# Performance work log

Measured on AMD Instinct MI355X. Metric: run time of the kernel, lower is better.

Reference implementation:

```python
import jax, jax.numpy as jnp
import numpy as np

N_QUBITS = 12
N_LAYERS = 6
N_CLASSES = 10
BATCH = 4096


def _rot_matrix(phi, theta, omega):
    # PennyLane Rot(phi, theta, omega) = RZ(omega) @ RY(theta) @ RZ(phi)
    ct = jnp.cos(theta / 2).astype(jnp.complex64)
    st = jnp.sin(theta / 2).astype(jnp.complex64)
    ep = jnp.exp(-0.5j * (phi + omega)).astype(jnp.complex64)  # e^{-i(phi+omega)/2}
    em = jnp.exp(-0.5j * (phi - omega)).astype(jnp.complex64)  # e^{-i(phi-omega)/2}
    row0 = jnp.stack([ep * ct, -jnp.conj(em) * st])
    row1 = jnp.stack([em * st, jnp.conj(ep) * ct])
    return jnp.stack([row0, row1])  # [2, 2] complex64


def _apply_1q(state, U, q):
    # state: [B] + [2]*n ; apply 2x2 gate U on qubit axis q
    s = jnp.moveaxis(state, q + 1, -1)
    s = jnp.einsum('...i,ji->...j', s, U)
    return jnp.moveaxis(s, -1, q + 1)


def _apply_cnot(state, c, t):
    # flip target axis where control bit == 1
    s = jnp.moveaxis(state, (c + 1, t + 1), (1, 2))
    s = jnp.concatenate([s[:, :1], jnp.flip(s[:, 1:2], axis=2)], axis=1)
    return jnp.moveaxis(s, (1, 2), (c + 1, t + 1))


def _pauliz_signs(n):
    idx = np.arange(2 ** n)
    bits = (idx[None, :] >> (n - 1 - np.arange(n))[:, None]) & 1  # [n, 2^n]
    return jnp.asarray(1.0 - 2.0 * bits, dtype=jnp.float32)


def _quantum_forward(x, q_params):
    B, n = x.shape
    # rotation encoding: RY(x_q)|0> = [cos(x/2), sin(x/2)] -> product state
    c = jnp.cos(x / 2)
    s = jnp.sin(x / 2)
    state = jnp.ones((B, 1), dtype=jnp.complex64)
    for q in range(n):
        amp = jnp.stack([c[:, q], s[:, q]], axis=-1).astype(jnp.complex64)  # [B, 2]
        state = (state[:, :, None] * amp[:, None, :]).reshape(B, -1)
    state = state.reshape((B,) + (2,) * n)
    # StronglyEntanglingLayers: per-layer Rot on every wire, then CNOT ring with range r
    for l in range(N_LAYERS):
        for q in range(n):
            U = _rot_matrix(q_params[l, q, 0], q_params[l, q, 1], q_params[l, q, 2])
            state = _apply_1q(state, U, q)
        r = (l % (n - 1)) + 1
        for q in range(n):
            state = _apply_cnot(state, q, (q + r) % n)
    probs = (jnp.abs(state) ** 2).reshape(B, -1).astype(jnp.float32)  # [B, 2^n]
    signs = _pauliz_signs(n)  # [n, 2^n]
    return probs @ signs.T  # PauliZ expvals, [B, n]


def setup_inputs() -> dict:
    key = jax.random.key(0)
    k1, k2, k3, k4 = jax.random.split(key, 4)
    x = jax.random.normal(k1, (BATCH, N_QUBITS), dtype=jnp.float32)
    q_params = 0.01 * jax.random.normal(k2, (N_LAYERS, N_QUBITS, 3), dtype=jnp.float32)
    lim = 1.0 / np.sqrt(N_QUBITS)
    fc_w = jax.random.uniform(k3, (N_CLASSES, N_QUBITS), jnp.float32, -lim, lim)
    fc_b = jax.random.uniform(k4, (N_CLASSES,), jnp.float32, -lim, lim)
    return {"x": x, "q_params": q_params, "fc_w": fc_w, "fc_b": fc_b}


def reference(x, q_params, fc_w, fc_b):
    expvals = _quantum_forward(x, q_params)  # [B, n_qubits]
    return expvals @ fc_w.T + fc_b  # logits [B, n_classes]
```

## Files before the change

kernel.cpp:

```cpp
#include <hip/hip_runtime.h>
#include <hip/hip_fp16.h>

#define NQ 12
#define NL 6
#define NC 10
#define DIM 4096
#define TPB 256
#define NPASS 18

typedef _Float16 half8_t __attribute__((ext_vector_type(8)));
typedef float f32x4 __attribute__((ext_vector_type(4)));
typedef unsigned u32;

struct PassT {
    u32 colL[4];
    u32 colW[2];
    u32 colT[2];
    u32 colS[4];
};
struct QCArgs {
    PassT P[NPASS];
    u32 GcolI[8], AcolI[8];
    u32 svoIlog[16], svoIaddr[16];
    u32 tidMask[NQ];
    u32 tab16[NQ];
};

__device__ __forceinline__ u32 packh2(float a, float b) {
    __half2 h;
    h.x = __float2half(a);
    h.y = __float2half(b);
    return __builtin_bit_cast(u32, h);
}
__device__ __forceinline__ float r16(float v) { return __half2float(__float2half(v)); }

__global__ __launch_bounds__(TPB) void prep_k(const float* __restrict__ qp, uint4* __restrict__ ws)
{
    __shared__ float4 gmat[NL * NQ];
    const unsigned tid = threadIdx.x;
    const unsigned lane = tid & 63;
    const unsigned wv = tid >> 6;

    if (tid < NL * NQ) {
        float phi = qp[tid * 3 + 0];
        float th  = qp[tid * 3 + 1];
        float om  = qp[tid * 3 + 2];
        float st_, ct, sa, ca, sb, cb;
        sincosf(0.5f * th, &st_, &ct);
        sincosf(0.5f * (phi + om), &sa, &ca);
        sincosf(0.5f * (phi - om), &sb, &cb);
        gmat[tid] = make_float4(ca * ct, -sa * ct, cb * st_, -sb * st_);
    }
    __syncthreads();

    const int i16 = lane & 15;
    const int sb0 = (int)(lane >> 4) * 4;
    for (int k = (int)wv; k < NPASS; k += 4) {
        const int gb = (k / 3) * NQ + (k % 3) * 4;
        u32 fH[4], fL[4];
        #pragma unroll
        for (int jj = 0; jj < 4; ++jj) {
            int s = sb0 + jj;
            float cre = 1.0f, cim = 0.0f;
            #pragma unroll
            for (int g = 0; g < 4; ++g) {
                float4 gq = gmat[gb + g];
                int ib = (i16 >> g) & 1, sb2 = (s >> g) & 1;
                float er, ei;
                if (ib == 0 && sb2 == 0)      { er =  gq.x; ei =  gq.y; }
                else if (ib == 0 && sb2 == 1) { er = -gq.z; ei =  gq.w; }
                else if (ib == 1 && sb2 == 0) { er =  gq.z; ei =  gq.w; }
                else                          { er =  gq.x; ei = -gq.y; }
                float nre = cre * er - cim * ei;
                float nim = cre * ei + cim * er;
                cre = nre; cim = nim;
            }
            float mi = -cim;
            fH[jj] = packh2(cre, mi);
            fL[jj] = packh2(cre - r16(cre), mi - r16(mi));
        }
        uint4 h = make_uint4(fH[0], fH[1], fH[2], fH[3]);
        uint4 l = make_uint4(fL[0], fL[1], fL[2], fL[3]);
        uint4 hI, lI;
        hI.x = ((h.x << 16) | (h.x >> 16)) ^ 0x8000u;
        hI.y = ((h.y << 16) | (h.y >> 16)) ^ 0x8000u;
        hI.z = ((h.z << 16) | (h.z >> 16)) ^ 0x8000u;
        hI.w = ((h.w << 16) | (h.w >> 16)) ^ 0x8000u;
        lI.x = ((l.x << 16) | (l.x >> 16)) ^ 0x8000u;
        lI.y = ((l.y << 16) | (l.y >> 16)) ^ 0x8000u;
        lI.z = ((l.z << 16) | (l.z >> 16)) ^ 0x8000u;
        lI.w = ((l.w << 16) | (l.w >> 16)) ^ 0x8000u;
        ws[0 * 1152 + k * 64 + lane] = h;
        ws[1 * 1152 + k * 64 + lane] = l;
        ws[2 * 1152 + k * 64 + lane] = hI;
        ws[3 * 1152 + k * 64 + lane] = lI;
    }
}

__global__ __launch_bounds__(TPB, 4) void qsim_k(
    const float* __restrict__ x,
    const float* __restrict__ fcw, const float* __restrict__ fcb,
    float* __restrict__ out, int B, const uint4* __restrict__ ws, QCArgs K)
{
    __shared__ u32 stamp[DIM];
    __shared__ float csn[NQ], snn[NQ];
    __shared__ float zred[4 * NQ];
    __shared__ float zfin[NQ];

    const unsigned tid = threadIdx.x;
    const unsigned lane = tid & 63;
    const unsigned wv = tid >> 6;
    const int blk = blockIdx.x;

    if (tid < NQ) {
        float s, c;
        sincosf(0.5f * x[(size_t)blk * NQ + tid], &s, &c);
        csn[tid] = c; snn[tid] = s;
    }
    __syncthreads();

    {
        float csr[NQ], snr[NQ];
        #pragma unroll
        for (int p = 0; p < NQ; ++p) { csr[p] = csn[11 - p]; snr[p] = snn[11 - p]; }
        u32 G = 0, A0 = 0;
        #pragma unroll
        for (int b = 0; b < 8; ++b) {
            u32 mneg = (u32)(-(int)((tid >> b) & 1u));
            G  ^= mneg & K.GcolI[b];
            A0 ^= mneg & K.AcolI[b];
        }
        #pragma unroll
        for (int s = 0; s < 16; ++s) {
            u32 idx = G ^ K.svoIlog[s];
            float amp = 1.0f;
            #pragma unroll
            for (int p = 0; p < NQ; ++p)
                amp *= ((idx >> p) & 1) ? snr[p] : csr[p];
            *(u32*)((char*)stamp + (A0 ^ K.svoIaddr[s])) = packh2(amp, 0.0f);
        }
    }

    float pr[16];

    #pragma unroll 1
    for (int k = 0; k < NPASS; ++k) {
        uint4 fh  = ws[0 * 1152 + k * 64 + lane];
        uint4 fl  = ws[1 * 1152 + k * 64 + lane];
        uint4 fhI = ws[2 * 1152 + k * 64 + lane];
        uint4 flI = ws[3 * 1152 + k * 64 + lane];
        half8_t AreH = __builtin_bit_cast(half8_t, fh);
        half8_t AreL = __builtin_bit_cast(half8_t, fl);
        half8_t AimH = __builtin_bit_cast(half8_t, fhI);
        half8_t AimL = __builtin_bit_cast(half8_t, flI);

        __syncthreads();
        const PassT& P = K.P[k];

        u32 A = 0;
        A ^= (lane & 1u)  ? P.colL[0] : 0u;
        A ^= (lane & 2u)  ? P.colL[1] : 0u;
        A ^= (lane & 4u)  ? P.colL[2] : 0u;
        A ^= (lane & 8u)  ? P.colL[3] : 0u;
        A ^= (lane & 16u) ? P.colS[2] : 0u;
        A ^= (lane & 32u) ? P.colS[3] : 0u;
        A ^= (wv & 1u) ? P.colW[0] : 0u;
        A ^= (wv & 2u) ? P.colW[1] : 0u;
        const u32 o1 = P.colS[0], o2 = P.colS[1], o3 = o1 ^ o2;
        const u32 t1 = P.colT[0], t2 = P.colT[1];
        const u32 tf[4] = {0u, t1, t2, t1 ^ t2};

        #pragma unroll
        for (int t = 0; t < 4; ++t) {
            u32 At = A ^ tf[t];
            u32 b0 = *(const u32*)((const char*)stamp + At);
            u32 b1 = *(const u32*)((const char*)stamp + (At ^ o1));
            u32 b2 = *(const u32*)((const char*)stamp + (At ^ o2));
            u32 b3 = *(const u32*)((const char*)stamp + (At ^ o3));
            half8_t Bf = __builtin_bit_cast(half8_t, make_uint4(b0, b1, b2, b3));
            f32x4 zc = {0.0f, 0.0f, 0.0f, 0.0f};
            f32x4 Dre = __builtin_amdgcn_mfma_f32_16x16x32_f16(
                AreH, Bf, __builtin_amdgcn_mfma_f32_16x16x32_f16(AreL, Bf, zc, 0, 0, 0), 0, 0, 0);
            f32x4 Dim = __builtin_amdgcn_mfma_f32_16x16x32_f16(
                AimH, Bf, __builtin_amdgcn_mfma_f32_16x16x32_f16(AimL, Bf, zc, 0, 0, 0), 0, 0, 0);
            if (k < NPASS - 1) {
                *(u32*)((char*)stamp + At)        = packh2(Dre[0], Dim[0]);
                *(u32*)((char*)stamp + (At ^ o1)) = packh2(Dre[1], Dim[1]);
                *(u32*)((char*)stamp + (At ^ o2)) = packh2(Dre[2], Dim[2]);
                *(u32*)((char*)stamp + (At ^ o3)) = packh2(Dre[3], Dim[3]);
            } else {
                pr[t * 4 + 0] = fmaf(Dre[0], Dre[0], Dim[0] * Dim[0]);
                pr[t * 4 + 1] = fmaf(Dre[1], Dre[1], Dim[1] * Dim[1]);
                pr[t * 4 + 2] = fmaf(Dre[2], Dre[2], Dim[2] * Dim[2]);
                pr[t * 4 + 3] = fmaf(Dre[3], Dre[3], Dim[3] * Dim[3]);
            }
        }
    }

    float z[NQ];
    #pragma unroll
    for (int q = 0; q < NQ; ++q) {
        float base = (__popc(K.tidMask[q] & tid) & 1) ? -1.0f : 1.0f;
        u32 tb = K.tab16[q];
        float acc = 0.0f;
        #pragma unroll
        for (int idx = 0; idx < 16; ++idx) {
            float sgn = ((tb >> idx) & 1u) ? -base : base;
            acc = fmaf(sgn, pr[idx], acc);
        }
        z[q] = acc;
    }
    #pragma unroll
    for (int q = 0; q < NQ; ++q) {
        float v = z[q];
        #pragma unroll
        for (int o = 1; o < 64; o <<= 1) v += __shfl_xor(v, o, 64);
        z[q] = v;
    }
    if ((tid & 63) == 0) {
        #pragma unroll
        for (int q = 0; q < NQ; ++q) zred[wv * NQ + q] = z[q];
    }
    __syncthreads();
    if (tid < NQ)
        zfin[tid] = zred[tid] + zred[NQ + tid] + zred[2 * NQ + tid] + zred[3 * NQ + tid];
    __syncthreads();

    if (tid < NC) {
        float acc = fcb[tid];
        #pragma unroll
        for (int q = 0; q < NQ; ++q) acc = fmaf(fcw[tid * NQ + q], zfin[q], acc);
        out[(size_t)blk * NC + tid] = acc;
    }
}

static void inv12(const unsigned Ain[12], unsigned Ai[12]) {
    unsigned M[12], I[12];
    for (int i = 0; i < 12; ++i) { M[i] = Ain[i]; I[i] = 1u << i; }
    for (int c = 0; c < 12; ++c) {
        int pr = -1;
        for (int r2 = c; r2 < 12; ++r2) if ((M[r2] >> c) & 1u) { pr = r2; break; }
        unsigned tm = M[c]; M[c] = M[pr]; M[pr] = tm;
        tm = I[c]; I[c] = I[pr]; I[pr] = tm;
        for (int r2 = 0; r2 < 12; ++r2)
            if (r2 != c && ((M[r2] >> c) & 1u)) { M[r2] ^= M[c]; I[r2] ^= I[c]; }
    }
    for (int i = 0; i < 12; ++i) Ai[i] = I[i];
}
static unsigned lcg(unsigned& s) { s = s * 1664525u + 1013904223u; return s >> 8; }
static int pc(unsigned v) { return __builtin_popcount(v); }

extern "C" void kernel_launch(void* const* d_in, const int* in_sizes, int n_in,
                              void* d_out, int out_size, void* d_ws, size_t ws_size,
                              hipStream_t stream) {
    const float* x    = (const float*)d_in[0];
    const float* qp   = (const float*)d_in[1];
    const float* fc_w = (const float*)d_in[2];
    const float* fc_b = (const float*)d_in[3];
    float* out = (float*)d_out;
    int B = in_sizes[0] / NQ;

    unsigned L[12];
    for (int i = 0; i < 12; ++i) L[i] = 1u << i;
    static unsigned vAll[NPASS][4], rAll[NPASS][4], vcAll[NPASS][16];
    static int posAll[NPASS][8];
    for (int l = 0; l < NL; ++l) {
        unsigned Linv[12];
        inv12(L, Linv);
        for (int m = 0; m < 3; ++m) {
            int k = l * 3 + m;
            for (int j = 0; j < 4; ++j) {
                int qq = 4 * m + j, bb = 11 - qq;
                rAll[k][j] = L[bb];
                unsigned vv = 0;
                for (int i = 0; i < 12; ++i) vv |= ((Linv[i] >> bb) & 1u) << i;
                vAll[k][j] = vv;
            }
            unsigned w[4]; int piv[4];
            for (int j = 0; j < 4; ++j) {
                w[j] = vAll[k][j];
                for (int k2 = 0; k2 < j; ++k2)
                    if ((w[j] >> piv[k2]) & 1u) w[j] ^= w[k2];
                piv[j] = __builtin_ctz(w[j]);
            }
            bool ispiv[12] = {};
            for (int j = 0; j < 4; ++j) ispiv[piv[j]] = true;
            int c = 0;
            for (int pos = 0; pos < 12; ++pos)
                if (!ispiv[pos]) posAll[k][c++] = pos;
            for (int s = 0; s < 16; ++s) {
                unsigned vc = 0;
                for (int j = 0; j < 4; ++j) if ((s >> j) & 1) vc ^= vAll[k][j];
                vcAll[k][s] = vc;
            }
        }
        int rr = l + 1;
        for (int q = 0; q < 12; ++q) {
            int tq = (q + rr) % 12;
            L[11 - tq] ^= L[11 - q];
        }
    }
    unsigned rfin[12];
    for (int q = 0; q < 12; ++q) rfin[q] = L[11 - q];

    unsigned labels[12];
    unsigned seed = 0x5EED321u;
    auto lab5 = [&](unsigned v) -> unsigned {
        unsigned r = 0;
        for (int pos = 0; pos < 12; ++pos) if ((v >> pos) & 1u) r ^= labels[pos];
        return r & 31u;
    };
    bool okAll = false;
    for (int att = 0; att < 300000 && !okAll; ++att) {
        for (int i = 0; i < 12; ++i) labels[i] = 1u + (lcg(seed) % 31u);
        okAll = true;
        for (int k = 0; k < NPASS && okAll; ++k) {
            unsigned Labj[4];
            for (int j = 0; j < 4; ++j) Labj[j] = lab5(vAll[k][j]);
            unsigned ech[5], low[5]; int rk = 0;
            unsigned v2l = Labj[2];
            if (v2l) { ech[rk] = v2l; low[rk] = v2l & (0u - v2l); ++rk; }
            int got = 0;
            for (int b = 0; b < 8 && got < 4; ++b) {
                int p = posAll[k][b];
                unsigned f = labels[p] & 31u;
                for (int j = 0; j < 4; ++j) if ((rAll[k][j] >> p) & 1u) f ^= Labj[j];
                unsigned vv = f & 31u;
                for (int i = 0; i < rk; ++i) if (vv & low[i]) vv ^= ech[i];
                if (vv) { ech[rk] = vv; low[rk] = vv & (0u - vv); ++rk; ++got; }
            }
            okAll = (rk == 5);
        }
    }
    for (int k = 0; k < NPASS; ++k) {
        unsigned Labj[4];
        for (int j = 0; j < 4; ++j) Labj[j] = lab5(vAll[k][j]);
        unsigned ech[5], low[5]; int rk = 0;
        unsigned v2l = Labj[2];
        if (v2l) { ech[rk] = v2l; low[rk] = v2l & (0u - v2l); ++rk; }
        int used[8] = {}, chosen[4], nch = 0;
        for (int b = 0; b < 8 && nch < 4; ++b) {
            int p = posAll[k][b];
            unsigned f = labels[p] & 31u;
            for (int j = 0; j < 4; ++j) if ((rAll[k][j] >> p) & 1u) f ^= Labj[j];
            unsigned vv = f & 31u;
            for (int i = 0; i < rk; ++i) if (vv & low[i]) vv ^= ech[i];
            if (vv) { ech[rk] = vv; low[rk] = vv & (0u - vv); ++rk; chosen[nch++] = b; used[b] = 1; }
        }
        for (int b = 0; b < 8 && nch < 4; ++b)
            if (!used[b]) { chosen[nch++] = b; used[b] = 1; }
        int outp[8]; int c2 = 0;
        for (int j = 0; j < nch; ++j) outp[c2++] = posAll[k][chosen[j]];
        for (int b = 0; b < 8; ++b) if (!used[b]) outp[c2++] = posAll[k][b];
        for (int b = 0; b < 8; ++b) posAll[k][b] = outp[b];
    }

    unsigned Trow[12];
    {
        unsigned ech[12], low[12]; int rk = 0;
        auto addrow = [&](unsigned vr) -> bool {
            unsigned vv = vr;
            for (int i = 0; i < rk; ++i) if (vv & low[i]) vv ^= ech[i];
            if (!vv) return false;
            ech[rk] = vv; low[rk] = vv & (0u - vv); ++rk;
            return true;
        };
        int idx = 0;
        for (int i = 0; i < 5; ++i) {
            unsigned r = 0;
            for (int pos = 0; pos < 12; ++pos) r |= ((labels[pos] >> i) & 1u) << pos;
            if (addrow(r)) Trow[idx++] = r;
        }
        int tries = 0;
        while (idx < 12 && tries < 100000) {
            unsigned rr2 = lcg(seed) & 4095u;
            if (rr2 && addrow(rr2)) Trow[idx++] = rr2;
            ++tries;
        }
        for (int i = 0; i < 12 && idx < 12; ++i)
            if (addrow(1u << i)) Trow[idx++] = 1u << i;
    }
    unsigned Tcol[12];
    for (int pos = 0; pos < 12; ++pos) {
        unsigned o = 0;
        for (int i = 0; i < 12; ++i) o |= ((Trow[i] >> pos) & 1u) << i;
        Tcol[pos] = o;
    }
    auto Tmap = [&](unsigned m) -> unsigned {
        unsigned o = 0;
        for (int i = 0; i < 12; ++i) o |= (unsigned)(pc(Trow[i] & m) & 1) << i;
        return o;
    };

    QCArgs K;
    __builtin_memset(&K, 0, sizeof(K));
    for (int k = 0; k < NPASS; ++k) {
        unsigned Dt[4];
        for (int j = 0; j < 4; ++j) Dt[j] = Tmap(vAll[k][j]);
        auto foldcol = [&](int p) -> unsigned {
            unsigned col = Tcol[p];
            for (int j = 0; j < 4; ++j)
                if ((rAll[k][j] >> p) & 1u) col ^= Dt[j];
            return col << 2;
        };
        for (int b = 0; b < 4; ++b) K.P[k].colL[b] = foldcol(posAll[k][b]);
        K.P[k].colW[0] = foldcol(posAll[k][4]);
        K.P[k].colW[1] = foldcol(posAll[k][5]);
        K.P[k].colT[0] = foldcol(posAll[k][6]);
        K.P[k].colT[1] = foldcol(posAll[k][7]);
        for (int j = 0; j < 4; ++j) K.P[k].colS[j] = Dt[j] << 2;
    }
    for (int b = 0; b < 8; ++b) {
        int p = posAll[0][b];
        unsigned g2 = 1u << p;
        unsigned col = Tcol[p];
        for (int j = 0; j < 4; ++j) {
            if ((rAll[0][j] >> p) & 1u) {
                g2  ^= vAll[0][j];
                col ^= Tmap(vAll[0][j]);
            }
        }
        K.GcolI[b] = g2;
        K.AcolI[b] = col << 2;
    }
    for (int s = 0; s < 16; ++s) {
        K.svoIlog[s]  = vcAll[0][s];
        K.svoIaddr[s] = Tmap(vcAll[0][s]) << 2;
    }
    const int kl = NPASS - 1;
    for (int q = 0; q < NQ; ++q) {
        auto wsbit = [&](int p) -> unsigned {
            unsigned bit = (rfin[q] >> p) & 1u;
            for (int j = 0; j < 4; ++j)
                bit ^= ((rAll[kl][j] >> p) & 1u) & (unsigned)(pc(rfin[q] & vAll[kl][j]) & 1);
            return bit;
        };
        unsigned tm = 0;
        for (int b = 0; b < 4; ++b) tm |= wsbit(posAll[kl][b]) << b;
        tm |= (unsigned)(pc(rfin[q] & vAll[kl][2]) & 1) << 4;
        tm |= (unsigned)(pc(rfin[q] & vAll[kl][3]) & 1) << 5;
        tm |= wsbit(posAll[kl][4]) << 6;
        tm |= wsbit(posAll[kl][5]) << 7;
        K.tidMask[q] = tm;
        unsigned tb0 = wsbit(posAll[kl][6]), tb1 = wsbit(posAll[kl][7]);
        unsigned j0 = (unsigned)(pc(rfin[q] & vAll[kl][0]) & 1);
        unsigned j1 = (unsigned)(pc(rfin[q] & vAll[kl][1]) & 1);
        unsigned tab = 0;
        for (int t = 0; t < 4; ++t)
            for (int jj = 0; jj < 4; ++jj) {
                unsigned s2 = ((t & 1) ? tb0 : 0u) ^ ((t & 2) ? tb1 : 0u)
                            ^ ((jj & 1) ? j0 : 0u) ^ ((jj & 2) ? j1 : 0u);
                tab |= s2 << (t * 4 + jj);
            }
        K.tab16[q] = tab;
    }

    uint4* wsv = (uint4*)d_ws;
    prep_k<<<1, TPB, 0, stream>>>(qp, wsv);
    qsim_k<<<B, TPB, 0, stream>>>(x, fc_w, fc_b, out, B, wsv, K);
}
```

Baseline: 114.5 us.

## Fuse initial state build into first gate pass and use pkrtz conversions

The product-state amplitudes are now computed directly in registers as MFMA B operands for pass 0, which removes the initial LDS write, the barrier and the readback. Float-to-half packing switches to the hardware round-toward-zero pack instruction, and the gate matrices are scaled slightly to offset the rounding bias. The pass loop is fully unrolled, address masks are precomputed once per thread, and launch bounds are raised to 6 waves per SIMD. Round-toward-zero adds accuracy risk, and the higher occupancy target could force register spills.

```diff
diff --git a/kernel.cpp b/kernel.cpp
--- a/kernel.cpp
+++ b/kernel.cpp
@@ -9,6 +9,7 @@
 #define NPASS 18
 
 typedef _Float16 half8_t __attribute__((ext_vector_type(8)));
+typedef __fp16 fp16x2 __attribute__((ext_vector_type(2)));
 typedef float f32x4 __attribute__((ext_vector_type(4)));
 typedef unsigned u32;
 
@@ -20,12 +21,17 @@
 };
 struct QCArgs {
     PassT P[NPASS];
-    u32 GcolI[8], AcolI[8];
-    u32 svoIlog[16], svoIaddr[16];
+    u32 GcolP0[8];
+    u32 tLogP0[4];
+    u32 sLogP0[4];
     u32 tidMask[NQ];
     u32 tab16[NQ];
 };
 
+__device__ __forceinline__ u32 pkrtz(float a, float b) {
+    fp16x2 r = __builtin_amdgcn_cvt_pkrtz(a, b);
+    return __builtin_bit_cast(u32, r);
+}
 __device__ __forceinline__ u32 packh2(float a, float b) {
     __half2 h;
     h.x = __float2half(a);
@@ -40,6 +46,7 @@
     const unsigned tid = threadIdx.x;
     const unsigned lane = tid & 63;
     const unsigned wv = tid >> 6;
+    const float SCALE = 1.00048828125f;
 
     if (tid < NL * NQ) {
         float phi = qp[tid * 3 + 0];
@@ -75,7 +82,8 @@
                 float nim = cre * ei + cim * er;
                 cre = nre; cim = nim;
             }
-            float mi = -cim;
+            float mi = -cim * SCALE;
+            cre *= SCALE;
             fH[jj] = packh2(cre, mi);
             fL[jj] = packh2(cre - r16(cre), mi - r16(mi));
         }
@@ -97,7 +105,7 @@
     }
 }
 
-__global__ __launch_bounds__(TPB, 4) void qsim_k(
+__global__ __launch_bounds__(TPB, 6) void qsim_k(
     const float* __restrict__ x,
     const float* __restrict__ fcw, const float* __restrict__ fcb,
     float* __restrict__ out, int B, const uint4* __restrict__ ws, QCArgs K)
@@ -119,32 +127,64 @@
     }
     __syncthreads();
 
+    u32 mb[8];
+    #pragma unroll
+    for (int b = 0; b < 8; ++b) mb[b] = (u32)(-(int)((tid >> b) & 1u));
+
+    float pr[16];
+
     {
+        uint4 fh  = ws[0 * 1152 + lane];
+        uint4 fl  = ws[1 * 1152 + lane];
+        uint4 fhI = ws[2 * 1152 + lane];
+        uint4 flI = ws[3 * 1152 + lane];
+        half8_t AreH = __builtin_bit_cast(half8_t, fh);
+        half8_t AreL = __builtin_bit_cast(half8_t, fl);
+        half8_t AimH = __builtin_bit_cast(half8_t, fhI);
+        half8_t AimL = __builtin_bit_cast(half8_t, flI);
+
         float csr[NQ], snr[NQ];
         #pragma unroll
         for (int p = 0; p < NQ; ++p) { csr[p] = csn[11 - p]; snr[p] = snn[11 - p]; }
-        u32 G = 0, A0 = 0;
-        #pragma unroll
-        for (int b = 0; b < 8; ++b) {
-            u32 mneg = (u32)(-(int)((tid >> b) & 1u));
-            G  ^= mneg & K.GcolI[b];
-            A0 ^= mneg & K.AcolI[b];
-        }
-        #pragma unroll
-        for (int s = 0; s < 16; ++s) {
-            u32 idx = G ^ K.svoIlog[s];
-            float amp = 1.0f;
+        u32 Glog = 0;
+        #pragma unroll
+        for (int b = 0; b < 8; ++b) Glog ^= mb[b] & K.GcolP0[b];
+
+        const PassT& P = K.P[0];
+        u32 A = (mb[0] & P.colL[0]) ^ (mb[1] & P.colL[1]) ^ (mb[2] & P.colL[2]) ^ (mb[3] & P.colL[3])
+              ^ (mb[4] & P.colS[2]) ^ (mb[5] & P.colS[3]) ^ (mb[6] & P.colW[0]) ^ (mb[7] & P.colW[1]);
+        const u32 o1 = P.colS[0], o2 = P.colS[1], o3 = o1 ^ o2;
+        const u32 t1 = P.colT[0], t2 = P.colT[1];
+        const u32 tf[4] = {0u, t1, t2, t1 ^ t2};
+
+        #pragma unroll
+        for (int t = 0; t < 4; ++t) {
+            u32 bb[4];
             #pragma unroll
-            for (int p = 0; p < NQ; ++p)
-                amp *= ((idx >> p) & 1) ? snr[p] : csr[p];
-            *(u32*)((char*)stamp + (A0 ^ K.svoIaddr[s])) = packh2(amp, 0.0f);
-        }
-    }
-
-    float pr[16];
-
-    #pragma unroll 1
-    for (int k = 0; k < NPASS; ++k) {
+            for (int jj = 0; jj < 4; ++jj) {
+                u32 idx = Glog ^ K.tLogP0[t] ^ K.sLogP0[jj];
+                float amp = 1.0f;
+                #pragma unroll
+                for (int p = 0; p < NQ; ++p)
+                    amp *= ((idx >> p) & 1) ? snr[p] : csr[p];
+                bb[jj] = pkrtz(amp, 0.0f);
+            }
+            half8_t Bf = __builtin_bit_cast(half8_t, make_uint4(bb[0], bb[1], bb[2], bb[3]));
+            f32x4 zc = {0.0f, 0.0f, 0.0f, 0.0f};
+            f32x4 Dre = __builtin_amdgcn_mfma_f32_16x16x32_f16(
+                AreH, Bf, __builtin_amdgcn_mfma_f32_16x16x32_f16(AreL, Bf, zc, 0, 0, 0), 0, 0, 0);
+            f32x4 Dim = __builtin_amdgcn_mfma_f32_16x16x32_f16(
+                AimH, Bf, __builtin_amdgcn_mfma_f32_16x16x32_f16(AimL, Bf, zc, 0, 0, 0), 0, 0, 0);
+            u32 At = A ^ tf[t];
+            *(u32*)((char*)stamp + At)        = pkrtz(Dre[0], Dim[0]);
+            *(u32*)((char*)stamp + (At ^ o1)) = pkrtz(Dre[1], Dim[1]);
+            *(u32*)((char*)stamp + (At ^ o2)) = pkrtz(Dre[2], Dim[2]);
+            *(u32*)((char*)stamp + (At ^ o3)) = pkrtz(Dre[3], Dim[3]);
+        }
+    }
+
+    #pragma unroll
+    for (int k = 1; k < NPASS; ++k) {
         uint4 fh  = ws[0 * 1152 + k * 64 + lane];
         uint4 fl  = ws[1 * 1152 + k * 64 + lane];
         uint4 fhI = ws[2 * 1152 + k * 64 + lane];
@@ -156,16 +196,8 @@
 
         __syncthreads();
         const PassT& P = K.P[k];
-
-        u32 A = 0;
-        A ^= (lane & 1u)  ? P.colL[0] : 0u;
-        A ^= (lane & 2u)  ? P.colL[1] : 0u;
-        A ^= (lane & 4u)  ? P.colL[2] : 0u;
-        A ^= (lane & 8u)  ? P.colL[3] : 0u;
-        A ^= (lane & 16u) ? P.colS[2] : 0u;
-        A ^= (lane & 32u) ? P.colS[3] : 0u;
-        A ^= (wv & 1u) ? P.colW[0] : 0u;
-        A ^= (wv & 2u) ? P.colW[1] : 0u;
+        u32 A = (mb[0] & P.colL[0]) ^ (mb[1] & P.colL[1]) ^ (mb[2] & P.colL[2]) ^ (mb[3] & P.colL[3])
+              ^ (mb[4] & P.colS[2]) ^ (mb[5] & P.colS[3]) ^ (mb[6] & P.colW[0]) ^ (mb[7] & P.colW[1]);
         const u32 o1 = P.colS[0], o2 = P.colS[1], o3 = o1 ^ o2;
         const u32 t1 = P.colT[0], t2 = P.colT[1];
         const u32 tf[4] = {0u, t1, t2, t1 ^ t2};
@@ -184,10 +216,10 @@
             f32x4 Dim = __builtin_amdgcn_mfma_f32_16x16x32_f16(
                 AimH, Bf, __builtin_amdgcn_mfma_f32_16x16x32_f16(AimL, Bf, zc, 0, 0, 0), 0, 0, 0);
             if (k < NPASS - 1) {
-                *(u32*)((char*)stamp + At)        = packh2(Dre[0], Dim[0]);
-                *(u32*)((char*)stamp + (At ^ o1)) = packh2(Dre[1], Dim[1]);
-                *(u32*)((char*)stamp + (At ^ o2)) = packh2(Dre[2], Dim[2]);
-                *(u32*)((char*)stamp + (At ^ o3)) = packh2(Dre[3], Dim[3]);
+                *(u32*)((char*)stamp + At)        = pkrtz(Dre[0], Dim[0]);
+                *(u32*)((char*)stamp + (At ^ o1)) = pkrtz(Dre[1], Dim[1]);
+                *(u32*)((char*)stamp + (At ^ o2)) = pkrtz(Dre[2], Dim[2]);
+                *(u32*)((char*)stamp + (At ^ o3)) = pkrtz(Dre[3], Dim[3]);
             } else {
                 pr[t * 4 + 0] = fmaf(Dre[0], Dre[0], Dim[0] * Dim[0]);
                 pr[t * 4 + 1] = fmaf(Dre[1], Dre[1], Dim[1] * Dim[1]);
@@ -410,23 +442,16 @@
         K.P[k].colT[1] = foldcol(posAll[k][7]);
         for (int j = 0; j < 4; ++j) K.P[k].colS[j] = Dt[j] << 2;
     }
-    for (int b = 0; b < 8; ++b) {
-        int p = posAll[0][b];
-        unsigned g2 = 1u << p;
-        unsigned col = Tcol[p];
-        for (int j = 0; j < 4; ++j) {
-            if ((rAll[0][j] >> p) & 1u) {
-                g2  ^= vAll[0][j];
-                col ^= Tmap(vAll[0][j]);
-            }
-        }
-        K.GcolI[b] = g2;
-        K.AcolI[b] = col << 2;
-    }
-    for (int s = 0; s < 16; ++s) {
-        K.svoIlog[s]  = vcAll[0][s];
-        K.svoIaddr[s] = Tmap(vcAll[0][s]) << 2;
-    }
+    for (int b = 0; b < 4; ++b) K.GcolP0[b] = 1u << posAll[0][b];
+    K.GcolP0[4] = vAll[0][2];
+    K.GcolP0[5] = vAll[0][3];
+    K.GcolP0[6] = 1u << posAll[0][4];
+    K.GcolP0[7] = 1u << posAll[0][5];
+    for (int t = 0; t < 4; ++t)
+        K.tLogP0[t] = ((t & 1) ? (1u << posAll[0][6]) : 0u) ^ ((t & 2) ? (1u << posAll[0][7]) : 0u);
+    for (int jj = 0; jj < 4; ++jj)
+        K.sLogP0[jj] = ((jj & 1) ? vAll[0][0] : 0u) ^ ((jj & 2) ? vAll[0][1] : 0u);
+
     const int kl = NPASS - 1;
     for (int q = 0; q < NQ; ++q) {
         auto wsbit = [&](int p) -> unsigned {
```

New measurement: 102.8 us (median of 2 runs). -10.2%, faster.
